# Kernel tuning notes

Hardware: AMD Instinct MI355X
Metric: run time of the kernel (lower is better)

## Reference

```python
import jax, jax.numpy as jnp
import numpy as np

N_HEAD = 16

def setup_inputs() -> dict:
    key = jax.random.key(0)
    k1, k2, k3 = jax.random.split(key, 3)
    B, K, C = 2, 2048, 1024
    x = jax.random.normal(k1, (B, K, C), dtype=jnp.float32)
    W_qkv = jax.random.normal(k2, (C, 3 * C), dtype=jnp.float32) * (1.0 / np.sqrt(C))
    b_qkv = jnp.zeros((3 * C,), dtype=jnp.float32)
    W_proj = jax.random.normal(k3, (C, C), dtype=jnp.float32) * (1.0 / np.sqrt(C))
    b_proj = jnp.zeros((C,), dtype=jnp.float32)
    return {"x": x, "W_qkv": W_qkv, "b_qkv": b_qkv, "W_proj": W_proj, "b_proj": b_proj, "K": K}

def reference(x, W_qkv, b_qkv, W_proj, b_proj, K):
    B, _, C = x.shape
    H = N_HEAD
    Dh = C // H
    qkv = x @ W_qkv + b_qkv                      # [B, K, 3C]
    q, k, v = jnp.split(qkv, 3, axis=-1)
    # [B, H, K, Dh]
    q = q.reshape(B, K, H, Dh).transpose(0, 2, 1, 3)
    k = k.reshape(B, K, H, Dh).transpose(0, 2, 1, 3)
    v = v.reshape(B, K, H, Dh).transpose(0, 2, 1, 3)
    att = jnp.einsum('bhqd,bhkd->bhqk', q, k) / jnp.sqrt(jnp.asarray(Dh, dtype=x.dtype))
    causal = jnp.tril(jnp.ones((K, K), dtype=bool))
    att = jnp.where(causal[None, None], att, jnp.asarray(-jnp.inf, dtype=x.dtype))
    att = jax.nn.softmax(att, axis=-1)
    y = jnp.einsum('bhqk,bhkd->bhqd', att, v)    # [B, H, K, Dh]
    y = y.transpose(0, 2, 1, 3).reshape(B, K, C)
    return y @ W_proj + b_proj
```

## Files before the change

### kernel.cpp

```cpp
#include <hip/hip_runtime.h>
#include <hip/hip_bf16.h>
#include <math.h>

typedef __attribute__((ext_vector_type(8))) short short8;
typedef __attribute__((ext_vector_type(4))) float f32x4;
typedef __attribute__((ext_vector_type(4))) short short4v;
typedef __attribute__((ext_vector_type(2))) int int2v;

static __device__ __forceinline__ short f2bf(float f) {
    __hip_bfloat16 h = __float2bfloat16(f);
    return *reinterpret_cast<short*>(&h);
}
static __device__ __forceinline__ void store_out(float* p, float v) { *p = v; }
static __device__ __forceinline__ void store_out(short* p, float v) { *p = f2bf(v); }

#define GLL16(g, l) __builtin_amdgcn_global_load_lds( \
    (const __attribute__((address_space(1))) void*)(g), \
    (__attribute__((address_space(3))) void*)(l), 16, 0, 0)

#if __has_builtin(__builtin_amdgcn_exp2f)
#define EXP2(x) __builtin_amdgcn_exp2f(x)
#else
#define EXP2(x) exp2f(x)
#endif

#if __has_builtin(__builtin_amdgcn_cvt_pk_bf16_f32)
typedef __attribute__((ext_vector_type(2))) __bf16 bf16x2;
static __device__ __forceinline__ int pack2bf(float a, float b) {
    bf16x2 r = __builtin_amdgcn_cvt_pk_bf16_f32(a, b);
    return __builtin_bit_cast(int, r);
}
#else
static __device__ __forceinline__ int pack2bf(float a, float b) {
    unsigned ua = __builtin_bit_cast(unsigned, a) + 0x8000u;
    unsigned ub = __builtin_bit_cast(unsigned, b) + 0x8000u;
    return (int)((ua >> 16) | (ub & 0xFFFF0000u));
}
#endif

struct BTrue  { static constexpr bool v = true;  };
struct BFalse { static constexpr bool v = false; };

static __device__ __forceinline__ void transpose_cast_tile(
    const float* __restrict__ W, short* __restrict__ Wt, int Kd, int N,
    int bx, int by)
{
    __shared__ float ts[32][33];
    const int c0 = bx * 32, r0 = by * 32;
    const int tx = threadIdx.x & 31, ty = threadIdx.x >> 5;
    #pragma unroll
    for (int e = 0; e < 4; ++e)
        ts[ty + e * 8][tx] = W[(size_t)(r0 + ty + e * 8) * N + c0 + tx];
    __syncthreads();
    #pragma unroll
    for (int e = 0; e < 4; ++e)
        Wt[(size_t)(c0 + ty + e * 8) * Kd + r0 + tx] = f2bf(ts[tx][ty + e * 8]);
}

__global__ __launch_bounds__(256) void prep_kernel(
    const float* __restrict__ x,      short* __restrict__ xb,    int nx,
    const float* __restrict__ W_qkv,  short* __restrict__ Wt1,
    const float* __restrict__ W_proj, short* __restrict__ Wt2,
    int C)
{
    const int nbx = nx / 1024;
    const int nb1 = (3 * C / 32) * (C / 32);
    int bid = blockIdx.x;
    if (bid < nbx) {
        int i = (bid * 256 + threadIdx.x) * 4;
        float4 v = *(const float4*)(x + i);
        short4v o = { f2bf(v.x), f2bf(v.y), f2bf(v.z), f2bf(v.w) };
        *(short4v*)(xb + i) = o;
        return;
    }
    bid -= nbx;
    if (bid < nb1) {
        const int nc = 3 * C / 32;
        transpose_cast_tile(W_qkv, Wt1, C, 3 * C, bid % nc, bid / nc);
        return;
    }
    bid -= nb1;
    {
        const int nc = C / 32;
        transpose_cast_tile(W_proj, Wt2, C, C, bid % nc, bid / nc);
    }
}

__global__ __launch_bounds__(256) void vtrans_kernel(
    const short* __restrict__ qkvb, short* __restrict__ vt, int K, int C)
{
    __shared__ short Vs[64][72];
    const int k0 = blockIdx.x * 64, h = blockIdx.y, b = blockIdx.z;
    const size_t rs = (size_t)3 * C;
    const short* src = qkvb + (size_t)b * K * rs + 2 * C + h * 64;
    const int key = threadIdx.x >> 3, d0 = (threadIdx.x & 7) * 8;
    *(short8*)&Vs[key][d0]      = *(const short8*)(src + (size_t)(k0 + key) * rs + d0);
    *(short8*)&Vs[key + 32][d0] = *(const short8*)(src + (size_t)(k0 + key + 32) * rs + d0);
    __syncthreads();
    const int d = threadIdx.x >> 2, kc = threadIdx.x & 3;
    short* dst = vt + ((size_t)(b * 16 + h) * 64 + d) * K + k0 + kc * 16;
    short8 o0, o1;
    #pragma unroll
    for (int j = 0; j < 8; ++j) { o0[j] = Vs[kc * 16 + j][d]; o1[j] = Vs[kc * 16 + 8 + j][d]; }
    *(short8*)dst = o0;
    *(short8*)(dst + 8) = o1;
}

#define GM 128
#define GN 128
#define GK 32

template <typename OutT>
__global__ __launch_bounds__(256) void gemm_mfma_kernel(
    const short* __restrict__ A, const short* __restrict__ Bt,
    const float* __restrict__ bias, OutT* __restrict__ C,
    int M, int N, int Kd, int qcols, float qscale)
{
    __shared__ __attribute__((aligned(16))) short As[GM * GK];
    __shared__ __attribute__((aligned(16))) short Bs[GN * GK];
    const int tid  = threadIdx.x;
    const int lane = tid & 63, w = tid >> 6;
    const int col  = lane & 15, quad = lane >> 4;
    const int wm = (w & 1) * 64, wn = (w >> 1) * 64;
    const int row0 = blockIdx.y * GM, col0 = blockIdx.x * GN;
    const float sc = (col0 < qcols) ? qscale : 1.f;

    const int sr = tid >> 2, scg = (tid & 3) * 8;
    const short* gA = A  + (size_t)(row0 + sr) * Kd + scg;
    const short* gB = Bt + (size_t)(col0 + sr) * Kd + scg;
    short* lA = As + sr * GK + scg;
    short* lB = Bs + sr * GK + scg;
    const size_t skip = (size_t)64 * Kd;

    f32x4 acc[4][4] = {};
    for (int k0 = 0; k0 < Kd; k0 += GK) {
        __syncthreads();
        GLL16(gA,        lA);
        GLL16(gA + skip, lA + 64 * GK);
        GLL16(gB,        lB);
        GLL16(gB + skip, lB + 64 * GK);
        gA += GK; gB += GK;
        __syncthreads();

        short8 aF[4], bF[4];
        #pragma unroll
        for (int mt = 0; mt < 4; ++mt)
            aF[mt] = *(const short8*)&As[(wm + mt * 16 + col) * GK + quad * 8];
        #pragma unroll
        for (int nt = 0; nt < 4; ++nt)
            bF[nt] = *(const short8*)&Bs[(wn + nt * 16 + col) * GK + quad * 8];
        #pragma unroll
        for (int mt = 0; mt < 4; ++mt)
            #pragma unroll
            for (int nt = 0; nt < 4; ++nt)
                acc[mt][nt] = __builtin_amdgcn_mfma_f32_16x16x32_bf16(aF[mt], bF[nt], acc[mt][nt], 0, 0, 0);
    }

    #pragma unroll
    for (int mt = 0; mt < 4; ++mt)
        #pragma unroll
        for (int i = 0; i < 4; ++i) {
            const size_t r = row0 + wm + mt * 16 + quad * 4 + i;
            #pragma unroll
            for (int nt = 0; nt < 4; ++nt) {
                const int c = col0 + wn + nt * 16 + col;
                store_out(&C[r * N + c], (acc[mt][nt][i] + bias[c]) * sc);
            }
        }
}

#define DH 64
#define FKT 64

__global__ __launch_bounds__(128) void flash_mfma_kernel(
    const short* __restrict__ qkvb,
    const short* __restrict__ vt,
    short* __restrict__ y,
    int K, int C)
{
    __shared__ __attribute__((aligned(16))) short Ks2[2 * 64 * 32];
    __shared__ __attribute__((aligned(16))) short Vs2[2 * 64 * 32];
    __shared__ __attribute__((aligned(16))) short Pt[2][32][72];

    const int tid  = threadIdx.x;
    const int lane = tid & 63, w = tid >> 6;
    const int col  = lane & 15, quad = lane >> 4;

    const int cmb  = blockIdx.x & 31;
    const int g    = blockIdx.x >> 5;
    const int b    = cmb >> 4, h = cmb & 15;
    const int NT   = K / 64;

    short8 bOnes;
    #pragma unroll
    for (int j = 0; j < 8; ++j) bOnes[j] = (col == 0) ? (short)0x3F80 : (short)0;

    const size_t rs = (size_t)3 * C;
    const short* qbase = qkvb + (size_t)b * K * rs + h * DH;
    const short* kbase = qbase + C;
    const short* vbase = vt + (size_t)(b * 16 + h) * DH * K;

    auto run = [&](int t0) {
        const int q0 = t0 + w * 32;

        short8 aQ[2][2];
        #pragma unroll
        for (int qg = 0; qg < 2; ++qg) {
            const short* qp = qbase + (size_t)(q0 + qg * 16 + col) * rs;
            aQ[qg][0] = *(const short8*)(qp + quad * 8);
            aQ[qg][1] = *(const short8*)(qp + 32 + quad * 8);
        }
        f32x4 O[2][4] = {};
        f32x4 L4[2] = {};

        const int nkt = t0 / FKT + 1;
        for (int it = 0; it < nkt; ++it) {
            const int kt = it * FKT;
            __syncthreads();
            #pragma unroll
            for (int cc = 0; cc < 4; ++cc) {
                const int seg  = w * 4 + cc;
                const int half = seg >> 2, kseg = seg & 3;
                const int rowl = kseg * 16 + (lane >> 2);
                const int grow = rowl ^ ((rowl >> 2) & 3);
                const int off  = half * 32 + (lane & 3) * 8;
                GLL16(kbase + (size_t)(kt + grow) * rs + off, &Ks2[seg * 512 + lane * 8]);
                GLL16(vbase + (size_t)rowl * K + kt + off,    &Vs2[seg * 512 + lane * 8]);
            }
            __syncthreads();

            short8 bK[4][2], bV[4][2];
            #pragma unroll
            for (int nb = 0; nb < 4; ++nb) {
                const int prow = (col * 4 + nb) ^ (col & 3);
                bK[nb][0] = *(const short8*)&Ks2[prow * 32 + quad * 8];
                bK[nb][1] = *(const short8*)&Ks2[2048 + prow * 32 + quad * 8];
            }
            #pragma unroll
            for (int db = 0; db < 4; ++db) {
                bV[db][0] = *(const short8*)&Vs2[(db * 16 + col) * 32 + quad * 8];
                bV[db][1] = *(const short8*)&Vs2[2048 + (db * 16 + col) * 32 + quad * 8];
            }

            #pragma unroll
            for (int qg = 0; qg < 2; ++qg) {
                const int qb = q0 + qg * 16;

                f32x4 S[4] = {};
                #pragma unroll
                for (int nb = 0; nb < 4; ++nb) {
                    S[nb] = __builtin_amdgcn_mfma_f32_16x16x32_bf16(aQ[qg][0], bK[nb][0], S[nb], 0, 0, 0);
                    S[nb] = __builtin_amdgcn_mfma_f32_16x16x32_bf16(aQ[qg][1], bK[nb][1], S[nb], 0, 0, 0);
                }

                auto smax = [&](auto tag) {
                    constexpr bool MASKED = decltype(tag)::v;
                    #pragma unroll
                    for (int i = 0; i < 4; ++i) {
                        const int q = qb + quad * 4 + i;
                        float sv0 = S[0][i], sv1 = S[1][i], sv2 = S[2][i], sv3 = S[3][i];
                        if constexpr (MASKED) {
                            const int kc4 = kt + col * 4;
                            sv0 = (kc4 + 0 <= q) ? sv0 : -INFINITY;
                            sv1 = (kc4 + 1 <= q) ? sv1 : -INFINITY;
                            sv2 = (kc4 + 2 <= q) ? sv2 : -INFINITY;
                            sv3 = (kc4 + 3 <= q) ? sv3 : -INFINITY;
                        }
                        const float p0 = EXP2(sv0);
                        const float p1 = EXP2(sv1);
                        const float p2 = EXP2(sv2);
                        const float p3 = EXP2(sv3);
                        int2v pw = { pack2bf(p0, p1), pack2bf(p2, p3) };
                        *(int2v*)&Pt[w][qg * 16 + quad * 4 + i][col * 4] = pw;
                    }
                };
                if (kt + 63 <= qb) smax(BFalse{}); else smax(BTrue{});

                asm volatile("s_waitcnt lgkmcnt(0)" ::: "memory");

                #pragma unroll
                for (int half = 0; half < 2; ++half) {
                    short8 aP = *(const short8*)&Pt[w][qg * 16 + col][half * 32 + quad * 8];
                    #pragma unroll
                    for (int db = 0; db < 4; ++db)
                        O[qg][db] = __builtin_amdgcn_mfma_f32_16x16x32_bf16(aP, bV[db][half], O[qg][db], 0, 0, 0);
                    L4[qg] = __builtin_amdgcn_mfma_f32_16x16x32_bf16(aP, bOnes, L4[qg], 0, 0, 0);
                }
            }
        }

        #pragma unroll
        for (int qg = 0; qg < 2; ++qg)
            #pragma unroll
            for (int i = 0; i < 4; ++i) {
                const float l = __shfl(L4[qg][i], quad * 16, 64);
                const float inv = 1.f / l;
                const int q = q0 + qg * 16 + quad * 4 + i;
                short* yr = y + ((size_t)b * K + q) * C + h * DH;
                #pragma unroll
                for (int db = 0; db < 4; ++db)
                    yr[db * 16 + col] = f2bf(O[qg][db][i] * inv);
            }
    };

    run(g * 64);
    run((NT - 1 - g) * 64);
}

extern "C" void kernel_launch(void* const* d_in, const int* in_sizes, int n_in,
                              void* d_out, int out_size, void* d_ws, size_t ws_size,
                              hipStream_t stream)
{
    const float* x      = (const float*)d_in[0];
    const float* W_qkv  = (const float*)d_in[1];
    const float* b_qkv  = (const float*)d_in[2];
    const float* W_proj = (const float*)d_in[3];
    const float* b_proj = (const float*)d_in[4];

    const int B = 2, K = 2048, C = 1024, H = 16;
    const int M = B * K;
    const float C2 = 0.18033688f;

    char* ws = (char*)d_ws;
    short* xb    = (short*)ws;  ws += (size_t)M * C * 2;
    short* Wt1   = (short*)ws;  ws += (size_t)3 * C * C * 2;
    short* Wt2   = (short*)ws;  ws += (size_t)C * C * 2;
    short* qkvb  = (short*)ws;  ws += (size_t)M * 3 * C * 2;
    short* yb    = (short*)ws;  ws += (size_t)M * C * 2;
    short* vtb   = (short*)ws;

    const int nbx = (M * C) / 1024;
    const int nb1 = (3 * C / 32) * (C / 32);
    const int nb2 = (C / 32) * (C / 32);
    prep_kernel<<<nbx + nb1 + nb2, 256, 0, stream>>>(x, xb, M * C, W_qkv, Wt1, W_proj, Wt2, C);

    dim3 g1((3 * C) / GN, M / GM);
    gemm_mfma_kernel<short><<<g1, 256, 0, stream>>>(xb, Wt1, b_qkv, qkvb, M, 3 * C, C, C, C2);

    dim3 gv(K / 64, H, B);
    vtrans_kernel<<<gv, 256, 0, stream>>>(qkvb, vtb, K, C);

    const int NPAIR = (K / 64) / 2;
    flash_mfma_kernel<<<dim3(NPAIR * 32), 128, 0, stream>>>(qkvb, vtb, yb, K, C);

    dim3 g3(C / GN, M / GM);
    gemm_mfma_kernel<float><<<g3, 256, 0, stream>>>(yb, Wt2, b_proj, (float*)d_out, M, C, C, 0, 1.f);
}
```

Measured before the change: 207.3 us.

## Split attention key chunks across four waves with LDS reduction of partial outputs

The flash attention kernel now uses 256 threads per block. Each wave handles all 64 query rows of a tile but only every fourth key chunk, loading its own K/V chunk into a private LDS region with no block-wide barriers inside the key loop. Partial O and row sums from the four waves are summed serially through LDS and then normalized and written out. This drops the per-iteration __syncthreads and spreads the work of the causal key range across waves. It adds a serialized four-step reduction, more LDS use (about 74KB), and per-wave load imbalance when a tile has few key chunks.

```diff
diff --git a/kernel.cpp b/kernel.cpp
--- a/kernel.cpp
+++ b/kernel.cpp
@@ -37,9 +37,6 @@
     return (int)((ua >> 16) | (ub & 0xFFFF0000u));
 }
 #endif
-
-struct BTrue  { static constexpr bool v = true;  };
-struct BFalse { static constexpr bool v = false; };
 
 static __device__ __forceinline__ void transpose_cast_tile(
     const float* __restrict__ W, short* __restrict__ Wt, int Kd, int N,
@@ -170,26 +167,27 @@
 }
 
 #define DH 64
-#define FKT 64
-
-__global__ __launch_bounds__(128) void flash_mfma_kernel(
+
+__global__ __launch_bounds__(256, 2) void flash_mfma_kernel(
     const short* __restrict__ qkvb,
     const short* __restrict__ vt,
     short* __restrict__ y,
     int K, int C)
 {
-    __shared__ __attribute__((aligned(16))) short Ks2[2 * 64 * 32];
-    __shared__ __attribute__((aligned(16))) short Vs2[2 * 64 * 32];
-    __shared__ __attribute__((aligned(16))) short Pt[2][32][72];
+    __shared__ __attribute__((aligned(16))) short smem[37888];
 
     const int tid  = threadIdx.x;
     const int lane = tid & 63, w = tid >> 6;
     const int col  = lane & 15, quad = lane >> 4;
 
-    const int cmb  = blockIdx.x & 31;
-    const int g    = blockIdx.x >> 5;
-    const int b    = cmb >> 4, h = cmb & 15;
-    const int NT   = K / 64;
+    short* Ksw = smem + w * 4160;
+    short* Vsw = smem + 16640 + w * 4160;
+    short* Ptw = smem + 33280 + w * 1152;
+    float* Or  = (float*)smem;
+
+    const int cmb = blockIdx.x & 31;
+    const int g   = blockIdx.x >> 5;
+    const int b   = cmb >> 4, h = cmb & 15;
 
     short8 bOnes;
     #pragma unroll
@@ -200,87 +198,79 @@
     const short* kbase = qbase + C;
     const short* vbase = vt + (size_t)(b * 16 + h) * DH * K;
 
-    auto run = [&](int t0) {
-        const int q0 = t0 + w * 32;
-
-        short8 aQ[2][2];
-        #pragma unroll
-        for (int qg = 0; qg < 2; ++qg) {
-            const short* qp = qbase + (size_t)(q0 + qg * 16 + col) * rs;
+    const int srow = lane & 56;
+    const int goff = (lane & 7) * 8;
+    const int loff = lane * 8;
+
+    auto run = [&](int T) {
+        const int t0 = T * 64;
+
+        short8 aQ[4][2];
+        #pragma unroll
+        for (int qg = 0; qg < 4; ++qg) {
+            const short* qp = qbase + (size_t)(t0 + qg * 16 + col) * rs;
             aQ[qg][0] = *(const short8*)(qp + quad * 8);
             aQ[qg][1] = *(const short8*)(qp + 32 + quad * 8);
         }
-        f32x4 O[2][4] = {};
-        f32x4 L4[2] = {};
-
-        const int nkt = t0 / FKT + 1;
-        for (int it = 0; it < nkt; ++it) {
-            const int kt = it * FKT;
-            __syncthreads();
-            #pragma unroll
-            for (int cc = 0; cc < 4; ++cc) {
-                const int seg  = w * 4 + cc;
-                const int half = seg >> 2, kseg = seg & 3;
-                const int rowl = kseg * 16 + (lane >> 2);
-                const int grow = rowl ^ ((rowl >> 2) & 3);
-                const int off  = half * 32 + (lane & 3) * 8;
-                GLL16(kbase + (size_t)(kt + grow) * rs + off, &Ks2[seg * 512 + lane * 8]);
-                GLL16(vbase + (size_t)rowl * K + kt + off,    &Vs2[seg * 512 + lane * 8]);
-            }
-            __syncthreads();
+        f32x4 O[4][4] = {};
+        f32x4 L4[4] = {};
+
+        for (int ci = w; ci <= T; ci += 4) {
+            const int kc = ci * 64;
+            #pragma unroll
+            for (int c2 = 0; c2 < 8; ++c2) {
+                GLL16(kbase + (size_t)(kc + srow + c2) * rs + goff, Ksw + c2 * 520 + loff);
+                GLL16(vbase + (size_t)(srow + c2) * K + kc + goff,  Vsw + c2 * 520 + loff);
+            }
+            asm volatile("s_waitcnt vmcnt(0)" ::: "memory");
 
             short8 bK[4][2], bV[4][2];
             #pragma unroll
             for (int nb = 0; nb < 4; ++nb) {
-                const int prow = (col * 4 + nb) ^ (col & 3);
-                bK[nb][0] = *(const short8*)&Ks2[prow * 32 + quad * 8];
-                bK[nb][1] = *(const short8*)&Ks2[2048 + prow * 32 + quad * 8];
+                const int ka = (4 * (col & 1) + nb) * 520 + (col >> 1) * 64 + quad * 8;
+                bK[nb][0] = *(const short8*)&Ksw[ka];
+                bK[nb][1] = *(const short8*)&Ksw[ka + 32];
             }
             #pragma unroll
             for (int db = 0; db < 4; ++db) {
-                bV[db][0] = *(const short8*)&Vs2[(db * 16 + col) * 32 + quad * 8];
-                bV[db][1] = *(const short8*)&Vs2[2048 + (db * 16 + col) * 32 + quad * 8];
-            }
-
-            #pragma unroll
-            for (int qg = 0; qg < 2; ++qg) {
-                const int qb = q0 + qg * 16;
-
+                const int va = (col & 7) * 520 + (db * 2 + (col >> 3)) * 64 + quad * 8;
+                bV[db][0] = *(const short8*)&Vsw[va];
+                bV[db][1] = *(const short8*)&Vsw[va + 32];
+            }
+
+            const bool diag = (kc == t0);
+            #pragma unroll
+            for (int qg = 0; qg < 4; ++qg) {
                 f32x4 S[4] = {};
                 #pragma unroll
                 for (int nb = 0; nb < 4; ++nb) {
                     S[nb] = __builtin_amdgcn_mfma_f32_16x16x32_bf16(aQ[qg][0], bK[nb][0], S[nb], 0, 0, 0);
                     S[nb] = __builtin_amdgcn_mfma_f32_16x16x32_bf16(aQ[qg][1], bK[nb][1], S[nb], 0, 0, 0);
                 }
-
-                auto smax = [&](auto tag) {
-                    constexpr bool MASKED = decltype(tag)::v;
+                if (!diag) {
                     #pragma unroll
                     for (int i = 0; i < 4; ++i) {
-                        const int q = qb + quad * 4 + i;
-                        float sv0 = S[0][i], sv1 = S[1][i], sv2 = S[2][i], sv3 = S[3][i];
-                        if constexpr (MASKED) {
-                            const int kc4 = kt + col * 4;
-                            sv0 = (kc4 + 0 <= q) ? sv0 : -INFINITY;
-                            sv1 = (kc4 + 1 <= q) ? sv1 : -INFINITY;
-                            sv2 = (kc4 + 2 <= q) ? sv2 : -INFINITY;
-                            sv3 = (kc4 + 3 <= q) ? sv3 : -INFINITY;
-                        }
-                        const float p0 = EXP2(sv0);
-                        const float p1 = EXP2(sv1);
-                        const float p2 = EXP2(sv2);
-                        const float p3 = EXP2(sv3);
-                        int2v pw = { pack2bf(p0, p1), pack2bf(p2, p3) };
-                        *(int2v*)&Pt[w][qg * 16 + quad * 4 + i][col * 4] = pw;
+                        int2v pw = { pack2bf(EXP2(S[0][i]), EXP2(S[1][i])),
+                                     pack2bf(EXP2(S[2][i]), EXP2(S[3][i])) };
+                        *(int2v*)&Ptw[(quad * 4 + i) * 72 + col * 4] = pw;
                     }
-                };
-                if (kt + 63 <= qb) smax(BFalse{}); else smax(BTrue{});
-
+                } else {
+                    const int qrel = qg * 16 + quad * 4;
+                    #pragma unroll
+                    for (int i = 0; i < 4; ++i) {
+                        float s0 = (col * 4 + 0 <= qrel + i) ? S[0][i] : -INFINITY;
+                        float s1 = (col * 4 + 1 <= qrel + i) ? S[1][i] : -INFINITY;
+                        float s2 = (col * 4 + 2 <= qrel + i) ? S[2][i] : -INFINITY;
+                        float s3 = (col * 4 + 3 <= qrel + i) ? S[3][i] : -INFINITY;
+                        int2v pw = { pack2bf(EXP2(s0), EXP2(s1)),
+                                     pack2bf(EXP2(s2), EXP2(s3)) };
+                        *(int2v*)&Ptw[(quad * 4 + i) * 72 + col * 4] = pw;
+                    }
+                }
                 asm volatile("s_waitcnt lgkmcnt(0)" ::: "memory");
-
                 #pragma unroll
                 for (int half = 0; half < 2; ++half) {
-                    short8 aP = *(const short8*)&Pt[w][qg * 16 + col][half * 32 + quad * 8];
+                    short8 aP = *(const short8*)&Ptw[col * 72 + half * 32 + quad * 8];
                     #pragma unroll
                     for (int db = 0; db < 4; ++db)
                         O[qg][db] = __builtin_amdgcn_mfma_f32_16x16x32_bf16(aP, bV[db][half], O[qg][db], 0, 0, 0);
@@ -289,22 +279,43 @@
             }
         }
 
-        #pragma unroll
-        for (int qg = 0; qg < 2; ++qg)
-            #pragma unroll
-            for (int i = 0; i < 4; ++i) {
-                const float l = __shfl(L4[qg][i], quad * 16, 64);
-                const float inv = 1.f / l;
-                const int q = q0 + qg * 16 + quad * 4 + i;
-                short* yr = y + ((size_t)b * K + q) * C + h * DH;
+        __syncthreads();
+        for (int ww = 0; ww < 4; ++ww) {
+            if (w == ww) {
                 #pragma unroll
-                for (int db = 0; db < 4; ++db)
-                    yr[db * 16 + col] = f2bf(O[qg][db][i] * inv);
-            }
+                for (int qg = 0; qg < 4; ++qg)
+                    #pragma unroll
+                    for (int i = 0; i < 4; ++i) {
+                        const int row = qg * 16 + quad * 4 + i;
+                        #pragma unroll
+                        for (int db = 0; db < 4; ++db) {
+                            float v = O[qg][db][i];
+                            if (ww == 0) Or[row * 68 + db * 16 + col] = v;
+                            else         Or[row * 68 + db * 16 + col] += v;
+                        }
+                        if (col == 0) {
+                            if (ww == 0) Or[row * 68 + 64] = L4[qg][i];
+                            else         Or[row * 68 + 64] += L4[qg][i];
+                        }
+                    }
+            }
+            __syncthreads();
+        }
+
+        #pragma unroll
+        for (int rstep = 0; rstep < 4; ++rstep) {
+            const int row = w * 16 + rstep * 4 + quad;
+            f32x4 ov = *(const f32x4*)&Or[row * 68 + col * 4];
+            const float inv = 1.f / Or[row * 68 + 64];
+            int2v o2 = { pack2bf(ov[0] * inv, ov[1] * inv),
+                         pack2bf(ov[2] * inv, ov[3] * inv) };
+            *(int2v*)(y + ((size_t)b * K + t0 + row) * C + h * DH + col * 4) = o2;
+        }
+        __syncthreads();
     };
 
-    run(g * 64);
-    run((NT - 1 - g) * 64);
+    run(g);
+    run(31 - g);
 }
 
 extern "C" void kernel_launch(void* const* d_in, const int* in_sizes, int n_in,
@@ -341,7 +352,7 @@
     vtrans_kernel<<<gv, 256, 0, stream>>>(qkvb, vtb, K, C);
 
     const int NPAIR = (K / 64) / 2;
-    flash_mfma_kernel<<<dim3(NPAIR * 32), 128, 0, stream>>>(qkvb, vtb, yb, K, C);
+    flash_mfma_kernel<<<dim3(NPAIR * 32), 256, 0, stream>>>(qkvb, vtb, yb, K, C);
 
     dim3 g3(C / GN, M / GM);
     gemm_mfma_kernel<float><<<g3, 256, 0, stream>>>(yb, Wt2, b_proj, (float*)d_out, M, C, C, 0, 1.f);
```

Measured after the change: 192.9 us. 7.0% less time.
